# Optimization experiments

Hardware: AMD Instinct MI355X
Metric: run time of the kernel (lower is better)

Reference implementation:

```python
import jax, jax.numpy as jnp
import numpy as np

N_NODES = 50000


def setup_inputs() -> dict:
    key = jax.random.key(0)
    k1, k2, k3, k4 = jax.random.split(key, 4)
    N, E, F_IN, F_OUT = N_NODES, 1600000, 512, 128
    x = jax.random.normal(k1, (N, F_IN), dtype=jnp.float32)
    edge_index = jax.random.randint(k2, (2, E), 0, N, dtype=jnp.int64)
    edge_weight = jax.random.uniform(k3, (E,), dtype=jnp.float32)
    # glorot init for weight, zeros bias (as in the original layer)
    limit = np.sqrt(6.0 / (F_IN + F_OUT)).astype(np.float32)
    weight = jax.random.uniform(k4, (F_IN, F_OUT), dtype=jnp.float32,
                                minval=-limit, maxval=limit)
    bias = jnp.zeros((F_OUT,), dtype=jnp.float32)
    return {"x": x, "edge_index": edge_index, "edge_weight": edge_weight,
            "weight": weight, "bias": bias}


def reference(x, edge_index, edge_weight, weight, bias):
    # dropout rate is 0 in this config -> identity
    h = x @ weight                                # [N, F_out] dense transform
    src, dst = edge_index[0], edge_index[1]
    # support @ h : sparse adjacency aggregation (SpMM) via gather + segment_sum
    msgs = h[src] * edge_weight[:, None]          # [E, F_out]
    agg = jax.ops.segment_sum(msgs, dst, num_segments=N_NODES)  # [N, F_out]
    return jax.nn.relu(agg + bias)
```

## Files before the change

### kernel.cpp

```cpp
#include <hip/hip_runtime.h>

#define F_IN  512
#define F_OUT 128
#define CB    128
#define EPB   4096
#define CMAX  512
#define CAP   8192

typedef __attribute__((ext_vector_type(8))) short  short8;
typedef __attribute__((ext_vector_type(4))) float  floatx4;

__device__ __forceinline__ unsigned short f2bf(float f) {
    unsigned u = __float_as_uint(f);
    return (unsigned short)((u + 0x7FFF + ((u >> 16) & 1)) >> 16);
}
__device__ __forceinline__ float bf2f(unsigned b) {
    return __uint_as_float(b << 16);
}

__global__ __launch_bounds__(256, 2) void gemm_mfma(
    const float* __restrict__ x, const unsigned short* __restrict__ wt,
    unsigned short* __restrict__ h, int N)
{
    __shared__ unsigned short sa[64 * 68];
    __shared__ unsigned short sb[128 * 68];

    const int tid  = threadIdx.x;
    const int wave = tid >> 6, lane = tid & 63;
    const int g    = lane >> 4, l16 = lane & 15;
    const int m0   = blockIdx.x * 64;

    const int arow = tid >> 2, aq = tid & 3;
    const int brow = tid >> 1, bh = tid & 1;

    floatx4 acc[8];
    #pragma unroll
    for (int i = 0; i < 8; ++i) acc[i] = (floatx4)(0.f);

    const bool  avalid = (m0 + arow) < N;
    const float* xp = x + (size_t)(m0 + arow) * F_IN + aq * 16;
    const unsigned short* bp = wt + brow * F_IN + bh * 32;

    float4 ax[4];
    uint4  bv[4];
    #pragma unroll
    for (int i = 0; i < 4; ++i) ax[i] = make_float4(0.f, 0.f, 0.f, 0.f);
    if (avalid) {
        #pragma unroll
        for (int i = 0; i < 4; ++i) ax[i] = ((const float4*)xp)[i];
    }
    #pragma unroll
    for (int i = 0; i < 4; ++i) bv[i] = ((const uint4*)bp)[i];

    for (int s = 0; s < 8; ++s) {
        __syncthreads();
        #pragma unroll
        for (int i = 0; i < 4; ++i) {
            ushort4 t;
            t.x = f2bf(ax[i].x); t.y = f2bf(ax[i].y);
            t.z = f2bf(ax[i].z); t.w = f2bf(ax[i].w);
            *(ushort4*)&sa[arow * 68 + aq * 16 + i * 4] = t;
        }
        #pragma unroll
        for (int i = 0; i < 4; ++i) {
            *(uint2*)&sb[brow * 68 + bh * 32 + i * 8]     = make_uint2(bv[i].x, bv[i].y);
            *(uint2*)&sb[brow * 68 + bh * 32 + i * 8 + 4] = make_uint2(bv[i].z, bv[i].w);
        }
        if (s < 7) {
            int k0n = (s + 1) * 64;
            if (avalid) {
                #pragma unroll
                for (int i = 0; i < 4; ++i) ax[i] = ((const float4*)(xp + k0n))[i];
            }
            #pragma unroll
            for (int i = 0; i < 4; ++i) bv[i] = ((const uint4*)(bp + k0n))[i];
        }
        __syncthreads();

        #pragma unroll
        for (int kc = 0; kc < 2; ++kc) {
            union { ushort4 u[2]; short8 v; } af;
            int abase = (wave * 16 + l16) * 68 + kc * 32 + g * 8;
            af.u[0] = *(ushort4*)&sa[abase];
            af.u[1] = *(ushort4*)&sa[abase + 4];
            #pragma unroll
            for (int nt = 0; nt < 8; ++nt) {
                union { ushort4 u[2]; short8 v; } bf;
                int bbase = (nt * 16 + l16) * 68 + kc * 32 + g * 8;
                bf.u[0] = *(ushort4*)&sb[bbase];
                bf.u[1] = *(ushort4*)&sb[bbase + 4];
                acc[nt] = __builtin_amdgcn_mfma_f32_16x16x32_bf16(af.v, bf.v, acc[nt], 0, 0, 0);
            }
        }
    }

    #pragma unroll
    for (int nt = 0; nt < 8; ++nt) {
        #pragma unroll
        for (int r = 0; r < 4; ++r) {
            int row = m0 + wave * 16 + g * 4 + r;
            if (row < N) h[(size_t)row * F_OUT + nt * 16 + l16] = f2bf(acc[nt][r]);
        }
    }
}

__global__ __launch_bounds__(512) void coarse_hist(
    const int* __restrict__ ei, int* __restrict__ cnt, int E, int C)
{
    __shared__ int lh[CMAX];
    int tid = threadIdx.x;
    if (tid < CMAX) lh[tid] = 0;
    __syncthreads();
    int base = blockIdx.x * EPB;
    #pragma unroll
    for (int j = 0; j < EPB / 512; ++j) {
        int e = base + j * 512 + tid;
        if (e < E) atomicAdd(&lh[ei[E + e] >> 7], 1);
    }
    __syncthreads();
    if (tid < C && lh[tid] > 0) atomicAdd(&cnt[tid], lh[tid]);
}

__global__ __launch_bounds__(512) void scan_convert(
    const int* __restrict__ cnt, int* __restrict__ binoff,
    int* __restrict__ cursor, int C, int E,
    const float* __restrict__ w, unsigned short* __restrict__ wt)
{
    if (blockIdx.x > 0) {
        int gid = (blockIdx.x - 1) * 512 + threadIdx.x;
        int n = gid >> 9, k = gid & 511;
        wt[gid] = f2bf(w[(size_t)k * F_OUT + n]);
        return;
    }
    __shared__ int s[CMAX];
    int tid = threadIdx.x;
    int v = (tid < C) ? cnt[tid] : 0;
    s[tid] = v;
    __syncthreads();
    #pragma unroll
    for (int off = 1; off < CMAX; off <<= 1) {
        int t = (tid >= off) ? s[tid - off] : 0;
        __syncthreads();
        s[tid] += t;
        __syncthreads();
    }
    if (tid < C) { int ex = s[tid] - v; binoff[tid] = ex; cursor[tid] = ex; }
    if (tid == 0) binoff[C] = E;
}

__global__ __launch_bounds__(512) void coarse_fill(
    const int* __restrict__ ei, const float* __restrict__ ew,
    int* __restrict__ cursor, unsigned* __restrict__ k32,
    unsigned char* __restrict__ d8, int E, int C)
{
    __shared__ int lh[CMAX];
    __shared__ int lbase[CMAX];
    int tid = threadIdx.x;
    if (tid < CMAX) lh[tid] = 0;
    __syncthreads();

    const int base = blockIdx.x * EPB;
    unsigned       mykey[EPB / 512];
    unsigned char  mydl[EPB / 512];
    short          mybin[EPB / 512];
    unsigned short myrank[EPB / 512];

    #pragma unroll
    for (int j = 0; j < EPB / 512; ++j) {
        int e = base + j * 512 + tid;
        mybin[j] = -1;
        if (e < E) {
            int   src = ei[e];
            int   dst = ei[E + e];
            float w   = ew[e];
            int bin = dst >> 7;
            mykey[j]  = (unsigned)src | ((unsigned)f2bf(w) << 16);
            mydl[j]   = (unsigned char)(dst & (CB - 1));
            mybin[j]  = (short)bin;
            myrank[j] = (unsigned short)atomicAdd(&lh[bin], 1);
        }
    }
    __syncthreads();
    if (tid < C && lh[tid] > 0) lbase[tid] = atomicAdd(&cursor[tid], lh[tid]);
    __syncthreads();
    #pragma unroll
    for (int j = 0; j < EPB / 512; ++j) {
        if (mybin[j] >= 0) {
            int p = lbase[mybin[j]] + myrank[j];
            k32[p] = mykey[j];
            d8[p]  = mydl[j];
        }
    }
}

__global__ __launch_bounds__(512) void fine_agg(
    const unsigned short* __restrict__ h, const unsigned* __restrict__ k32,
    const unsigned char* __restrict__ d8, const int* __restrict__ binoff,
    const float* __restrict__ bias, float* __restrict__ out, int N)
{
    __shared__ unsigned char sd[CAP];
    __shared__ unsigned      ssort[CAP];
    __shared__ int lh[CB], ssum[CB], lcur[CB];
    __shared__ int sso[CB + 1];

    const int b     = blockIdx.x;
    const int tid   = threadIdx.x;
    const int start = binoff[b];
    const int cnt   = binoff[b + 1] - start;
    const int wave  = tid >> 6;
    const int lane  = tid & 63;
    const int half  = lane >> 5;
    const int q     = lane & 31;
    const float4 bv = *(const float4*)&bias[q * 4];

    if (cnt <= CAP) {
        if (tid < CB) lh[tid] = 0;
        __syncthreads();
        for (int i = tid; i < cnt; i += 512) {
            unsigned char d = d8[start + i];
            sd[i] = d;
            atomicAdd(&lh[d], 1);
        }
        __syncthreads();
        if (tid < CB) ssum[tid] = lh[tid];
        __syncthreads();
        #pragma unroll
        for (int off = 1; off < CB; off <<= 1) {
            int t = 0;
            if (tid < CB && tid >= off) t = ssum[tid - off];
            __syncthreads();
            if (tid < CB) ssum[tid] += t;
            __syncthreads();
        }
        if (tid < CB) {
            int ex = ssum[tid] - lh[tid];
            sso[tid]  = ex;
            lcur[tid] = ex;
        }
        if (tid == 0) sso[CB] = cnt;
        __syncthreads();
        for (int i = tid; i < cnt; i += 512) {
            unsigned k = k32[start + i];
            int r = atomicAdd(&lcur[sd[i]], 1);
            ssort[r] = k;
        }
        __syncthreads();

        #pragma unroll 1
        for (int t = 0; t < 16; ++t) {
            int nd   = wave * 16 + t;
            int node = b * CB + nd;
            int s    = sso[nd], e = sso[nd + 1];
            float4 acc = make_float4(0.f, 0.f, 0.f, 0.f);
            for (int i = s; i < e; i += 8) {
                #pragma unroll
                for (int j = 0; j < 4; ++j) {
                    int idx = i + j * 2 + half;
                    unsigned bk = 0;
                    if (idx < e) bk = ssort[idx];
                    float wgt = bf2f(bk >> 16);
                    uint2 hv = *(const uint2*)&h[(size_t)(bk & 0xFFFF) * F_OUT + q * 4];
                    acc.x += bf2f(hv.x & 0xFFFF) * wgt;
                    acc.y += bf2f(hv.x >> 16)    * wgt;
                    acc.z += bf2f(hv.y & 0xFFFF) * wgt;
                    acc.w += bf2f(hv.y >> 16)    * wgt;
                }
            }
            acc.x += __shfl_xor(acc.x, 32);
            acc.y += __shfl_xor(acc.y, 32);
            acc.z += __shfl_xor(acc.z, 32);
            acc.w += __shfl_xor(acc.w, 32);
            if (half == 0 && node < N) {
                float4 o;
                o.x = fmaxf(acc.x + bv.x, 0.f);
                o.y = fmaxf(acc.y + bv.y, 0.f);
                o.z = fmaxf(acc.z + bv.z, 0.f);
                o.w = fmaxf(acc.w + bv.w, 0.f);
                *(float4*)&out[(size_t)node * F_OUT + q * 4] = o;
            }
        }
    } else {
        #pragma unroll 1
        for (int t = 0; t < 16; ++t) {
            int nd   = wave * 16 + t;
            int node = b * CB + nd;
            float4 acc = make_float4(0.f, 0.f, 0.f, 0.f);
            for (int i = 0; i < cnt; ++i) {
                if (d8[start + i] == (unsigned char)nd) {
                    unsigned bk = k32[start + i];
                    float wgt = bf2f(bk >> 16);
                    uint2 hv = *(const uint2*)&h[(size_t)(bk & 0xFFFF) * F_OUT + q * 4];
                    acc.x += bf2f(hv.x & 0xFFFF) * wgt;
                    acc.y += bf2f(hv.x >> 16)    * wgt;
                    acc.z += bf2f(hv.y & 0xFFFF) * wgt;
                    acc.w += bf2f(hv.y >> 16)    * wgt;
                }
            }
            if (half == 0 && node < N) {
                float4 o;
                o.x = fmaxf(acc.x + bv.x, 0.f);
                o.y = fmaxf(acc.y + bv.y, 0.f);
                o.z = fmaxf(acc.z + bv.z, 0.f);
                o.w = fmaxf(acc.w + bv.w, 0.f);
                *(float4*)&out[(size_t)node * F_OUT + q * 4] = o;
            }
        }
    }
}

static inline size_t align256(size_t x) { return (x + 255) & ~(size_t)255; }

extern "C" void kernel_launch(void* const* d_in, const int* in_sizes, int n_in,
                              void* d_out, int out_size, void* d_ws, size_t ws_size,
                              hipStream_t stream)
{
    const float* x    = (const float*)d_in[0];
    const int*   ei   = (const int*)  d_in[1];
    const float* ew   = (const float*)d_in[2];
    const float* w    = (const float*)d_in[3];
    const float* bias = (const float*)d_in[4];
    float*       out  = (float*)d_out;

    const int N = in_sizes[0] / F_IN;
    const int E = in_sizes[2];
    const int C = (N + CB - 1) / CB;

    char*  ws = (char*)d_ws;
    size_t off = 0;
    unsigned short* h      = (unsigned short*)(ws + off); off += align256((size_t)N * F_OUT * 2);
    unsigned short* wt     = (unsigned short*)(ws + off); off += align256((size_t)F_OUT * F_IN * 2);
    int*            cnt    = (int*)(ws + off);            off += align256((size_t)(C + 1) * 4);
    int*            binoff = (int*)(ws + off);            off += align256((size_t)(C + 1) * 4);
    int*            cursor = (int*)(ws + off);            off += align256((size_t)C * 4);
    unsigned*       k32    = (unsigned*)(ws + off);       off += align256((size_t)E * 4);
    unsigned char*  d8     = (unsigned char*)(ws + off);  off += align256((size_t)E);

    const int pblocks = (E + EPB - 1) / EPB;

    (void)hipMemsetAsync(cnt, 0, (size_t)C * 4, stream);
    coarse_hist<<<pblocks, 512, 0, stream>>>(ei, cnt, E, C);
    scan_convert<<<1 + (F_IN * F_OUT) / 512, 512, 0, stream>>>(cnt, binoff, cursor, C, E, w, wt);
    coarse_fill<<<pblocks, 512, 0, stream>>>(ei, ew, cursor, k32, d8, E, C);
    gemm_mfma<<<(N + 63) / 64, 256, 0, stream>>>(x, wt, h, N);
    fine_agg<<<C, 512, 0, stream>>>(h, k32, d8, binoff, bias, out, N);
}
```

Baseline: 280.9 us.

## Drop LDS staging in GEMM and split fine aggregation into half-bin blocks

The GEMM no longer stages tiles through shared memory. Each wave loads x rows and bf16 weight rows straight from global memory into MFMA operands, which removes barriers and LDS traffic but gives up reuse of B within the block and relies on the cache instead. The fine aggregation now launches two 256-thread blocks per 128-node bin, each handling 64 nodes. It uses a wave-shuffle scan and a smaller shared buffer, which raises block count and occupancy. The cost is that each block scans the full bin's d8 array twice.

```diff
diff --git a/kernel.cpp b/kernel.cpp
--- a/kernel.cpp
+++ b/kernel.cpp
@@ -5,7 +5,7 @@
 #define CB    128
 #define EPB   4096
 #define CMAX  512
-#define CAP   8192
+#define CAP   4096
 
 typedef __attribute__((ext_vector_type(8))) short  short8;
 typedef __attribute__((ext_vector_type(4))) float  floatx4;
@@ -17,80 +17,45 @@
 __device__ __forceinline__ float bf2f(unsigned b) {
     return __uint_as_float(b << 16);
 }
-
-__global__ __launch_bounds__(256, 2) void gemm_mfma(
+__device__ __forceinline__ unsigned pack2bf(float lo, float hi) {
+    return __builtin_amdgcn_perm(__float_as_uint(hi) + 0x8000u,
+                                 __float_as_uint(lo) + 0x8000u, 0x07060302u);
+}
+
+__global__ __launch_bounds__(256, 3) void gemm_direct(
     const float* __restrict__ x, const unsigned short* __restrict__ wt,
     unsigned short* __restrict__ h, int N)
 {
-    __shared__ unsigned short sa[64 * 68];
-    __shared__ unsigned short sb[128 * 68];
-
     const int tid  = threadIdx.x;
     const int wave = tid >> 6, lane = tid & 63;
     const int g    = lane >> 4, l16 = lane & 15;
-    const int m0   = blockIdx.x * 64;
-
-    const int arow = tid >> 2, aq = tid & 3;
-    const int brow = tid >> 1, bh = tid & 1;
+    const int m0   = blockIdx.x * 64 + wave * 16;
+
+    const int row  = m0 + l16;
+    const int rowc = min(row, N - 1);
+
+    const float*          xp = x  + (size_t)rowc * F_IN + g * 8;
+    const unsigned short* bp = wt + (size_t)l16 * F_IN + g * 8;
 
     floatx4 acc[8];
     #pragma unroll
     for (int i = 0; i < 8; ++i) acc[i] = (floatx4)(0.f);
 
-    const bool  avalid = (m0 + arow) < N;
-    const float* xp = x + (size_t)(m0 + arow) * F_IN + aq * 16;
-    const unsigned short* bp = wt + brow * F_IN + bh * 32;
-
-    float4 ax[4];
-    uint4  bv[4];
-    #pragma unroll
-    for (int i = 0; i < 4; ++i) ax[i] = make_float4(0.f, 0.f, 0.f, 0.f);
-    if (avalid) {
+    #pragma unroll
+    for (int kc = 0; kc < 16; ++kc) {
+        const int k0 = kc * 32;
+        float4 a0 = *(const float4*)(xp + k0);
+        float4 a1 = *(const float4*)(xp + k0 + 4);
+        union { unsigned u[4]; short8 v; } af;
+        af.u[0] = pack2bf(a0.x, a0.y);
+        af.u[1] = pack2bf(a0.z, a0.w);
+        af.u[2] = pack2bf(a1.x, a1.y);
+        af.u[3] = pack2bf(a1.z, a1.w);
         #pragma unroll
-        for (int i = 0; i < 4; ++i) ax[i] = ((const float4*)xp)[i];
-    }
-    #pragma unroll
-    for (int i = 0; i < 4; ++i) bv[i] = ((const uint4*)bp)[i];
-
-    for (int s = 0; s < 8; ++s) {
-        __syncthreads();
-        #pragma unroll
-        for (int i = 0; i < 4; ++i) {
-            ushort4 t;
-            t.x = f2bf(ax[i].x); t.y = f2bf(ax[i].y);
-            t.z = f2bf(ax[i].z); t.w = f2bf(ax[i].w);
-            *(ushort4*)&sa[arow * 68 + aq * 16 + i * 4] = t;
-        }
-        #pragma unroll
-        for (int i = 0; i < 4; ++i) {
-            *(uint2*)&sb[brow * 68 + bh * 32 + i * 8]     = make_uint2(bv[i].x, bv[i].y);
-            *(uint2*)&sb[brow * 68 + bh * 32 + i * 8 + 4] = make_uint2(bv[i].z, bv[i].w);
-        }
-        if (s < 7) {
-            int k0n = (s + 1) * 64;
-            if (avalid) {
-                #pragma unroll
-                for (int i = 0; i < 4; ++i) ax[i] = ((const float4*)(xp + k0n))[i];
-            }
-            #pragma unroll
-            for (int i = 0; i < 4; ++i) bv[i] = ((const uint4*)(bp + k0n))[i];
-        }
-        __syncthreads();
-
-        #pragma unroll
-        for (int kc = 0; kc < 2; ++kc) {
-            union { ushort4 u[2]; short8 v; } af;
-            int abase = (wave * 16 + l16) * 68 + kc * 32 + g * 8;
-            af.u[0] = *(ushort4*)&sa[abase];
-            af.u[1] = *(ushort4*)&sa[abase + 4];
-            #pragma unroll
-            for (int nt = 0; nt < 8; ++nt) {
-                union { ushort4 u[2]; short8 v; } bf;
-                int bbase = (nt * 16 + l16) * 68 + kc * 32 + g * 8;
-                bf.u[0] = *(ushort4*)&sb[bbase];
-                bf.u[1] = *(ushort4*)&sb[bbase + 4];
-                acc[nt] = __builtin_amdgcn_mfma_f32_16x16x32_bf16(af.v, bf.v, acc[nt], 0, 0, 0);
-            }
+        for (int nt = 0; nt < 8; ++nt) {
+            union { uint4 u; short8 v; } bf;
+            bf.u = *(const uint4*)(bp + (size_t)nt * 16 * F_IN + k0);
+            acc[nt] = __builtin_amdgcn_mfma_f32_16x16x32_bf16(af.v, bf.v, acc[nt], 0, 0, 0);
         }
     }
 
@@ -98,8 +63,9 @@
     for (int nt = 0; nt < 8; ++nt) {
         #pragma unroll
         for (int r = 0; r < 4; ++r) {
-            int row = m0 + wave * 16 + g * 4 + r;
-            if (row < N) h[(size_t)row * F_OUT + nt * 16 + l16] = f2bf(acc[nt][r]);
+            int orow = m0 + g * 4 + r;
+            if (orow < N)
+                h[(size_t)orow * F_OUT + nt * 16 + l16] = f2bf(acc[nt][r]);
         }
     }
 }
@@ -193,64 +159,66 @@
     }
 }
 
-__global__ __launch_bounds__(512) void fine_agg(
+__global__ __launch_bounds__(256) void fine_agg(
     const unsigned short* __restrict__ h, const unsigned* __restrict__ k32,
     const unsigned char* __restrict__ d8, const int* __restrict__ binoff,
     const float* __restrict__ bias, float* __restrict__ out, int N)
 {
-    __shared__ unsigned char sd[CAP];
-    __shared__ unsigned      ssort[CAP];
-    __shared__ int lh[CB], ssum[CB], lcur[CB];
-    __shared__ int sso[CB + 1];
+    __shared__ unsigned ssort[CAP];
+    __shared__ int lh[64], lcur[64];
+    __shared__ int sso[65];
 
     const int b     = blockIdx.x;
+    const int cb    = b >> 1;
+    const int hb    = b & 1;
     const int tid   = threadIdx.x;
-    const int start = binoff[b];
-    const int cnt   = binoff[b + 1] - start;
+    const int start = binoff[cb];
+    const int end   = binoff[cb + 1];
     const int wave  = tid >> 6;
     const int lane  = tid & 63;
     const int half  = lane >> 5;
     const int q     = lane & 31;
     const float4 bv = *(const float4*)&bias[q * 4];
 
-    if (cnt <= CAP) {
-        if (tid < CB) lh[tid] = 0;
-        __syncthreads();
-        for (int i = tid; i < cnt; i += 512) {
-            unsigned char d = d8[start + i];
-            sd[i] = d;
-            atomicAdd(&lh[d], 1);
-        }
-        __syncthreads();
-        if (tid < CB) ssum[tid] = lh[tid];
-        __syncthreads();
+    if (tid < 64) lh[tid] = 0;
+    __syncthreads();
+
+    for (int i = start + tid; i < end; i += 256) {
+        int d = d8[i];
+        if ((d >> 6) == hb) atomicAdd(&lh[d & 63], 1);
+    }
+    __syncthreads();
+
+    if (wave == 0) {
+        int v = lh[lane & 63];
+        int orig = v;
         #pragma unroll
-        for (int off = 1; off < CB; off <<= 1) {
-            int t = 0;
-            if (tid < CB && tid >= off) t = ssum[tid - off];
-            __syncthreads();
-            if (tid < CB) ssum[tid] += t;
-            __syncthreads();
-        }
-        if (tid < CB) {
-            int ex = ssum[tid] - lh[tid];
-            sso[tid]  = ex;
-            lcur[tid] = ex;
-        }
-        if (tid == 0) sso[CB] = cnt;
-        __syncthreads();
-        for (int i = tid; i < cnt; i += 512) {
-            unsigned k = k32[start + i];
-            int r = atomicAdd(&lcur[sd[i]], 1);
-            ssort[r] = k;
+        for (int off = 1; off < 64; off <<= 1) {
+            int t = __shfl_up(v, off);
+            if (lane >= off) v += t;
+        }
+        sso[lane]  = v - orig;
+        lcur[lane] = v - orig;
+        if (lane == 63) sso[64] = v;
+    }
+    __syncthreads();
+    const int hcnt = sso[64];
+
+    if (hcnt <= CAP) {
+        for (int i = start + tid; i < end; i += 256) {
+            int d = d8[i];
+            if ((d >> 6) == hb) {
+                int r = atomicAdd(&lcur[d & 63], 1);
+                ssort[r] = k32[i];
+            }
         }
         __syncthreads();
 
         #pragma unroll 1
         for (int t = 0; t < 16; ++t) {
             int nd   = wave * 16 + t;
-            int node = b * CB + nd;
-            int s    = sso[nd], e = sso[nd + 1];
+            int node = cb * CB + hb * 64 + nd;
+            int s = sso[nd], e = sso[nd + 1];
             float4 acc = make_float4(0.f, 0.f, 0.f, 0.f);
             for (int i = s; i < e; i += 8) {
                 #pragma unroll
@@ -283,11 +251,12 @@
         #pragma unroll 1
         for (int t = 0; t < 16; ++t) {
             int nd   = wave * 16 + t;
-            int node = b * CB + nd;
+            int node = cb * CB + hb * 64 + nd;
+            int want = hb * 64 + nd;
             float4 acc = make_float4(0.f, 0.f, 0.f, 0.f);
-            for (int i = 0; i < cnt; ++i) {
-                if (d8[start + i] == (unsigned char)nd) {
-                    unsigned bk = k32[start + i];
+            for (int i = start; i < end; ++i) {
+                if (d8[i] == (unsigned char)want) {
+                    unsigned bk = k32[i];
                     float wgt = bf2f(bk >> 16);
                     uint2 hv = *(const uint2*)&h[(size_t)(bk & 0xFFFF) * F_OUT + q * 4];
                     acc.x += bf2f(hv.x & 0xFFFF) * wgt;
@@ -341,6 +310,6 @@
     coarse_hist<<<pblocks, 512, 0, stream>>>(ei, cnt, E, C);
     scan_convert<<<1 + (F_IN * F_OUT) / 512, 512, 0, stream>>>(cnt, binoff, cursor, C, E, w, wt);
     coarse_fill<<<pblocks, 512, 0, stream>>>(ei, ew, cursor, k32, d8, E, C);
-    gemm_mfma<<<(N + 63) / 64, 256, 0, stream>>>(x, wt, h, N);
-    fine_agg<<<C, 512, 0, stream>>>(h, k32, d8, binoff, bias, out, N);
-}
+    gemm_direct<<<(N + 63) / 64, 256, 0, stream>>>(x, wt, h, N);
+    fine_agg<<<2 * C, 256, 0, stream>>>(h, k32, d8, binoff, bias, out, N);
+}
```

After: 322.5 us. 1.15x slower.

## Fuse fill with GEMM and hist with weight convert; split aggregation per half-bin

Applied to the files above, without the earlier changes.

The edge-fill partition and the bf16 MFMA GEMM now run as one launch, with block ranges split by block index so the two independent stages overlap. The weight transpose/convert also moves into the histogram launch. The per-edge key and destination offset are packed into one uint2 array instead of separate k32/d8 arrays. Fine aggregation now uses two 256-thread blocks per 128-node bin, each filtering its half of the nodes, so parallelism doubles and LDS use drops. The cost is that each half-block reads the full bin's entries, and entry storage grows to 8 bytes per edge.

```diff
diff --git a/kernel.cpp b/kernel.cpp
--- a/kernel.cpp
+++ b/kernel.cpp
@@ -5,7 +5,7 @@
 #define CB    128
 #define EPB   4096
 #define CMAX  512
-#define CAP   8192
+#define CAP   4096
 
 typedef __attribute__((ext_vector_type(8))) short  short8;
 typedef __attribute__((ext_vector_type(4))) float  floatx4;
@@ -18,17 +18,113 @@
     return __uint_as_float(b << 16);
 }
 
-__global__ __launch_bounds__(256, 2) void gemm_mfma(
+__global__ __launch_bounds__(256) void hist_convert(
+    const int* __restrict__ ei, int* __restrict__ cnt, int E, int C, int FB,
+    const float* __restrict__ w, unsigned short* __restrict__ wt)
+{
+    const int tid = threadIdx.x;
+    if ((int)blockIdx.x >= FB) {
+        int cid = blockIdx.x - FB;
+        int g0  = cid * 512 + tid;
+        #pragma unroll
+        for (int r = 0; r < 2; ++r) {
+            int gid = g0 + r * 256;
+            int n = gid >> 9, k = gid & 511;
+            wt[gid] = f2bf(w[(size_t)k * F_OUT + n]);
+        }
+        return;
+    }
+    __shared__ int lh[CMAX];
+    lh[tid] = 0; lh[tid + 256] = 0;
+    __syncthreads();
+    int base = blockIdx.x * EPB;
+    #pragma unroll
+    for (int j = 0; j < EPB / 256; ++j) {
+        int e = base + j * 256 + tid;
+        if (e < E) atomicAdd(&lh[ei[E + e] >> 7], 1);
+    }
+    __syncthreads();
+    if (tid < C && lh[tid] > 0) atomicAdd(&cnt[tid], lh[tid]);
+    int t2 = tid + 256;
+    if (t2 < C && lh[t2] > 0) atomicAdd(&cnt[t2], lh[t2]);
+}
+
+__global__ __launch_bounds__(512) void scan_bins(
+    const int* __restrict__ cnt, int* __restrict__ binoff,
+    int* __restrict__ cursor, int C, int E)
+{
+    __shared__ int s[CMAX];
+    int tid = threadIdx.x;
+    int v = (tid < C) ? cnt[tid] : 0;
+    s[tid] = v;
+    __syncthreads();
+    #pragma unroll
+    for (int off = 1; off < CMAX; off <<= 1) {
+        int t = (tid >= off) ? s[tid - off] : 0;
+        __syncthreads();
+        s[tid] += t;
+        __syncthreads();
+    }
+    if (tid < C) { int ex = s[tid] - v; binoff[tid] = ex; cursor[tid] = ex; }
+    if (tid == 0) binoff[C] = E;
+}
+
+__global__ __launch_bounds__(256, 2) void fill_gemm(
+    const int* __restrict__ ei, const float* __restrict__ ew,
+    int* __restrict__ cursor, uint2* __restrict__ ent, int E, int C, int FB,
     const float* __restrict__ x, const unsigned short* __restrict__ wt,
     unsigned short* __restrict__ h, int N)
 {
+    const int tid = threadIdx.x;
+
+    if ((int)blockIdx.x < FB) {
+        __shared__ int lh[CMAX];
+        __shared__ int lbase[CMAX];
+        lh[tid] = 0; lh[tid + 256] = 0;
+        __syncthreads();
+
+        const int base = blockIdx.x * EPB;
+        unsigned       mykey[EPB / 256];
+        unsigned char  mydl[EPB / 256];
+        short          mybin[EPB / 256];
+        unsigned short myrank[EPB / 256];
+
+        #pragma unroll
+        for (int j = 0; j < EPB / 256; ++j) {
+            int e = base + j * 256 + tid;
+            mybin[j] = -1;
+            if (e < E) {
+                int   src = ei[e];
+                int   dst = ei[E + e];
+                float w   = ew[e];
+                int bin = dst >> 7;
+                mykey[j]  = (unsigned)src | ((unsigned)f2bf(w) << 16);
+                mydl[j]   = (unsigned char)(dst & (CB - 1));
+                mybin[j]  = (short)bin;
+                myrank[j] = (unsigned short)atomicAdd(&lh[bin], 1);
+            }
+        }
+        __syncthreads();
+        if (tid < C && lh[tid] > 0) lbase[tid] = atomicAdd(&cursor[tid], lh[tid]);
+        int t2 = tid + 256;
+        if (t2 < C && lh[t2] > 0) lbase[t2] = atomicAdd(&cursor[t2], lh[t2]);
+        __syncthreads();
+        #pragma unroll
+        for (int j = 0; j < EPB / 256; ++j) {
+            if (mybin[j] >= 0) {
+                int p = lbase[mybin[j]] + myrank[j];
+                ent[p] = make_uint2(mykey[j], mydl[j]);
+            }
+        }
+        return;
+    }
+
     __shared__ unsigned short sa[64 * 68];
     __shared__ unsigned short sb[128 * 68];
 
-    const int tid  = threadIdx.x;
     const int wave = tid >> 6, lane = tid & 63;
     const int g    = lane >> 4, l16 = lane & 15;
-    const int m0   = blockIdx.x * 64;
+    const int m0   = (blockIdx.x - FB) * 64;
 
     const int arow = tid >> 2, aq = tid & 3;
     const int brow = tid >> 1, bh = tid & 1;
@@ -104,153 +200,67 @@
     }
 }
 
-__global__ __launch_bounds__(512) void coarse_hist(
-    const int* __restrict__ ei, int* __restrict__ cnt, int E, int C)
-{
-    __shared__ int lh[CMAX];
-    int tid = threadIdx.x;
-    if (tid < CMAX) lh[tid] = 0;
-    __syncthreads();
-    int base = blockIdx.x * EPB;
-    #pragma unroll
-    for (int j = 0; j < EPB / 512; ++j) {
-        int e = base + j * 512 + tid;
-        if (e < E) atomicAdd(&lh[ei[E + e] >> 7], 1);
-    }
-    __syncthreads();
-    if (tid < C && lh[tid] > 0) atomicAdd(&cnt[tid], lh[tid]);
-}
-
-__global__ __launch_bounds__(512) void scan_convert(
-    const int* __restrict__ cnt, int* __restrict__ binoff,
-    int* __restrict__ cursor, int C, int E,
-    const float* __restrict__ w, unsigned short* __restrict__ wt)
-{
-    if (blockIdx.x > 0) {
-        int gid = (blockIdx.x - 1) * 512 + threadIdx.x;
-        int n = gid >> 9, k = gid & 511;
-        wt[gid] = f2bf(w[(size_t)k * F_OUT + n]);
-        return;
-    }
-    __shared__ int s[CMAX];
-    int tid = threadIdx.x;
-    int v = (tid < C) ? cnt[tid] : 0;
-    s[tid] = v;
-    __syncthreads();
-    #pragma unroll
-    for (int off = 1; off < CMAX; off <<= 1) {
-        int t = (tid >= off) ? s[tid - off] : 0;
-        __syncthreads();
-        s[tid] += t;
-        __syncthreads();
-    }
-    if (tid < C) { int ex = s[tid] - v; binoff[tid] = ex; cursor[tid] = ex; }
-    if (tid == 0) binoff[C] = E;
-}
-
-__global__ __launch_bounds__(512) void coarse_fill(
-    const int* __restrict__ ei, const float* __restrict__ ew,
-    int* __restrict__ cursor, unsigned* __restrict__ k32,
-    unsigned char* __restrict__ d8, int E, int C)
-{
-    __shared__ int lh[CMAX];
-    __shared__ int lbase[CMAX];
-    int tid = threadIdx.x;
-    if (tid < CMAX) lh[tid] = 0;
-    __syncthreads();
-
-    const int base = blockIdx.x * EPB;
-    unsigned       mykey[EPB / 512];
-    unsigned char  mydl[EPB / 512];
-    short          mybin[EPB / 512];
-    unsigned short myrank[EPB / 512];
-
-    #pragma unroll
-    for (int j = 0; j < EPB / 512; ++j) {
-        int e = base + j * 512 + tid;
-        mybin[j] = -1;
-        if (e < E) {
-            int   src = ei[e];
-            int   dst = ei[E + e];
-            float w   = ew[e];
-            int bin = dst >> 7;
-            mykey[j]  = (unsigned)src | ((unsigned)f2bf(w) << 16);
-            mydl[j]   = (unsigned char)(dst & (CB - 1));
-            mybin[j]  = (short)bin;
-            myrank[j] = (unsigned short)atomicAdd(&lh[bin], 1);
-        }
-    }
-    __syncthreads();
-    if (tid < C && lh[tid] > 0) lbase[tid] = atomicAdd(&cursor[tid], lh[tid]);
-    __syncthreads();
-    #pragma unroll
-    for (int j = 0; j < EPB / 512; ++j) {
-        if (mybin[j] >= 0) {
-            int p = lbase[mybin[j]] + myrank[j];
-            k32[p] = mykey[j];
-            d8[p]  = mydl[j];
-        }
-    }
-}
-
-__global__ __launch_bounds__(512) void fine_agg(
-    const unsigned short* __restrict__ h, const unsigned* __restrict__ k32,
-    const unsigned char* __restrict__ d8, const int* __restrict__ binoff,
-    const float* __restrict__ bias, float* __restrict__ out, int N)
-{
-    __shared__ unsigned char sd[CAP];
-    __shared__ unsigned      ssort[CAP];
-    __shared__ int lh[CB], ssum[CB], lcur[CB];
-    __shared__ int sso[CB + 1];
+__global__ __launch_bounds__(256) void fine_agg(
+    const unsigned short* __restrict__ h, const uint2* __restrict__ ent,
+    const int* __restrict__ binoff, const float* __restrict__ bias,
+    float* __restrict__ out, int N)
+{
+    __shared__ unsigned ssort[CAP];
+    __shared__ int lh[64], lcur[64];
+    __shared__ int sso[65];
 
     const int b     = blockIdx.x;
+    const int cb    = b >> 1;
+    const int hb    = b & 1;
     const int tid   = threadIdx.x;
-    const int start = binoff[b];
-    const int cnt   = binoff[b + 1] - start;
+    const int start = binoff[cb];
+    const int end   = binoff[cb + 1];
     const int wave  = tid >> 6;
     const int lane  = tid & 63;
     const int half  = lane >> 5;
     const int q     = lane & 31;
     const float4 bv = *(const float4*)&bias[q * 4];
 
-    if (cnt <= CAP) {
-        if (tid < CB) lh[tid] = 0;
-        __syncthreads();
-        for (int i = tid; i < cnt; i += 512) {
-            unsigned char d = d8[start + i];
-            sd[i] = d;
-            atomicAdd(&lh[d], 1);
-        }
-        __syncthreads();
-        if (tid < CB) ssum[tid] = lh[tid];
-        __syncthreads();
-        #pragma unroll
-        for (int off = 1; off < CB; off <<= 1) {
-            int t = 0;
-            if (tid < CB && tid >= off) t = ssum[tid - off];
-            __syncthreads();
-            if (tid < CB) ssum[tid] += t;
-            __syncthreads();
-        }
-        if (tid < CB) {
-            int ex = ssum[tid] - lh[tid];
-            sso[tid]  = ex;
-            lcur[tid] = ex;
-        }
-        if (tid == 0) sso[CB] = cnt;
-        __syncthreads();
-        for (int i = tid; i < cnt; i += 512) {
-            unsigned k = k32[start + i];
-            int r = atomicAdd(&lcur[sd[i]], 1);
-            ssort[r] = k;
+    if (tid < 64) lh[tid] = 0;
+    __syncthreads();
+
+    for (int i = start + tid; i < end; i += 256) {
+        int d = (int)ent[i].y;
+        if ((d >> 6) == hb) atomicAdd(&lh[d & 63], 1);
+    }
+    __syncthreads();
+
+    if (wave == 0) {
+        int v = lh[lane & 63];
+        int orig = v;
+        #pragma unroll
+        for (int off = 1; off < 64; off <<= 1) {
+            int t = __shfl_up(v, off);
+            if (lane >= off) v += t;
+        }
+        sso[lane]  = v - orig;
+        lcur[lane] = v - orig;
+        if (lane == 63) sso[64] = v;
+    }
+    __syncthreads();
+    const int hcnt = sso[64];
+
+    if (hcnt <= CAP) {
+        for (int i = start + tid; i < end; i += 256) {
+            uint2 e = ent[i];
+            int d = (int)e.y;
+            if ((d >> 6) == hb) {
+                int r = atomicAdd(&lcur[d & 63], 1);
+                ssort[r] = e.x;
+            }
         }
         __syncthreads();
 
         #pragma unroll 1
         for (int t = 0; t < 16; ++t) {
             int nd   = wave * 16 + t;
-            int node = b * CB + nd;
-            int s    = sso[nd], e = sso[nd + 1];
+            int node = cb * CB + hb * 64 + nd;
+            int s = sso[nd], e = sso[nd + 1];
             float4 acc = make_float4(0.f, 0.f, 0.f, 0.f);
             for (int i = s; i < e; i += 8) {
                 #pragma unroll
@@ -283,11 +293,13 @@
         #pragma unroll 1
         for (int t = 0; t < 16; ++t) {
             int nd   = wave * 16 + t;
-            int node = b * CB + nd;
+            int node = cb * CB + hb * 64 + nd;
+            int want = hb * 64 + nd;
             float4 acc = make_float4(0.f, 0.f, 0.f, 0.f);
-            for (int i = 0; i < cnt; ++i) {
-                if (d8[start + i] == (unsigned char)nd) {
-                    unsigned bk = k32[start + i];
+            for (int i = start; i < end; ++i) {
+                uint2 e = ent[i];
+                if ((int)e.y == want) {
+                    unsigned bk = e.x;
                     float wgt = bf2f(bk >> 16);
                     uint2 hv = *(const uint2*)&h[(size_t)(bk & 0xFFFF) * F_OUT + q * 4];
                     acc.x += bf2f(hv.x & 0xFFFF) * wgt;
@@ -332,15 +344,16 @@
     int*            cnt    = (int*)(ws + off);            off += align256((size_t)(C + 1) * 4);
     int*            binoff = (int*)(ws + off);            off += align256((size_t)(C + 1) * 4);
     int*            cursor = (int*)(ws + off);            off += align256((size_t)C * 4);
-    unsigned*       k32    = (unsigned*)(ws + off);       off += align256((size_t)E * 4);
-    unsigned char*  d8     = (unsigned char*)(ws + off);  off += align256((size_t)E);
-
-    const int pblocks = (E + EPB - 1) / EPB;
+    uint2*          ent    = (uint2*)(ws + off);          off += align256((size_t)E * 8);
+
+    const int FB = (E + EPB - 1) / EPB;
+    const int GB = (N + 63) / 64;
+    const int WB = (F_IN * F_OUT) / 512;
 
     (void)hipMemsetAsync(cnt, 0, (size_t)C * 4, stream);
-    coarse_hist<<<pblocks, 512, 0, stream>>>(ei, cnt, E, C);
-    scan_convert<<<1 + (F_IN * F_OUT) / 512, 512, 0, stream>>>(cnt, binoff, cursor, C, E, w, wt);
-    coarse_fill<<<pblocks, 512, 0, stream>>>(ei, ew, cursor, k32, d8, E, C);
-    gemm_mfma<<<(N + 63) / 64, 256, 0, stream>>>(x, wt, h, N);
-    fine_agg<<<C, 512, 0, stream>>>(h, k32, d8, binoff, bias, out, N);
-}
+    hist_convert<<<FB + WB, 256, 0, stream>>>(ei, cnt, E, C, FB, w, wt);
+    scan_bins<<<1, 512, 0, stream>>>(cnt, binoff, cursor, C, E);
+    fill_gemm<<<FB + GB, 256, 0, stream>>>(ei, ew, cursor, ent, E, C, FB,
+                                           x, wt, h, N);
+    fine_agg<<<2 * C, 256, 0, stream>>>(h, ent, binoff, bias, out, N);
+}
```

Measured after the change: 271.6 us. -3.3%, faster.
